# Kernel tuning notes

Measured on AMD Instinct MI355X. Metric: run time of the kernel, lower is better.

The kernel has to match this reference:

```python
import jax, jax.numpy as jnp
import numpy as np

B, T, N, D, H = 16, 96, 325, 64, 64
BS = 1e-09  # bias init constant

def _xavier(key, shape):
    fan_in, fan_out = shape
    limit = float(np.sqrt(6.0 / (fan_in + fan_out)))
    return jax.random.uniform(key, shape, jnp.float32, -limit, limit)

def setup_inputs() -> dict:
    key = jax.random.key(0)
    k = jax.random.split(key, 6)
    return {
        "x": jax.random.normal(k[0], (B, T, N, D), jnp.float32),
        "o_s": jax.random.normal(k[1], (B, T, N, D), jnp.float32),
        "U_x": _xavier(k[2], (D, 4 * H)),
        "V_x": _xavier(k[3], (H, 4 * H)),
        "b_x": jnp.full((4 * H,), BS, jnp.float32),
        "U_g": _xavier(k[4], (D, 2 * H)),
        "V_g": _xavier(k[5], (H, 2 * H)),
        "b_g": jnp.full((2 * H,), BS, jnp.float32),
    }

def reference(x, o_s, U_x, V_x, b_x, U_g, V_g, b_g):
    b, t, n, d = x.shape
    h = V_x.shape[0]
    ht0 = jnp.zeros((b, n, h), x.dtype)
    ct0 = jnp.zeros((b, n, h), x.dtype)

    def step(carry, inp):
        ht, ct = carry
        xt, ost = inp  # [b, n, d] each
        gates = xt @ U_x + ht @ V_x + b_x          # [b, n, 4h]
        gov = jax.nn.sigmoid(ost @ U_g + ht @ V_g + b_g)  # [b, n, 2h]
        ft = jax.nn.sigmoid(gates[..., :h])
        it = jax.nn.sigmoid(gates[..., h:2 * h])
        ot = jax.nn.sigmoid(gates[..., 2 * h:3 * h])
        ut = jax.nn.sigmoid(gates[..., 3 * h:])
        gov_f = gov[..., :h]
        gov_u = gov[..., h:]
        ct = gov_f * ft * ct + gov_u * it * ut
        ht = ot * jnp.tanh(ct)
        return (ht, ct), ht

    xs = (jnp.swapaxes(x, 0, 1), jnp.swapaxes(o_s, 0, 1))  # time-major [t, b, n, d]
    (ht, ct), hseq = jax.lax.scan(step, (ht0, ct0), xs)
    hidden_seq = jnp.swapaxes(hseq, 0, 1)  # [b, t, n, h]
    return hidden_seq, ht, ct
```

## Files before the change

kernel.cpp:

```cpp
#include <hip/hip_runtime.h>
#include <stdint.h>


#define TT 96
#define NNROW 325
#define STEP_OFS 20800
#define HT_OFS 31948800
#define CT_OFS 32281600

typedef __attribute__((ext_vector_type(8))) short short8;
typedef __attribute__((ext_vector_type(4))) float f32x4;

#define BAR() asm volatile("s_waitcnt lgkmcnt(0)\n\ts_barrier" ::: "memory")

__device__ __forceinline__ short f2bf(float f) {
    union { float f; uint32_t u; } v; v.f = f;
    uint32_t r = (v.u + 0x7FFFu + ((v.u >> 16) & 1u)) >> 16;
    return (short)(r & 0xFFFFu);
}
__device__ __forceinline__ float frcp(float x) { return __builtin_amdgcn_rcpf(x); }
__device__ __forceinline__ float ex2(float x)  { return __builtin_amdgcn_exp2f(x); }
__device__ __forceinline__ uint32_t cvtpk(float lo, float hi) {
    uint32_t r;
    asm("v_cvt_pk_bf16_f32 %0, %1, %2" : "=v"(r) : "v"(lo), "v"(hi));
    return r;
}

__global__ __launch_bounds__(256, 2)
void glstm_kernel(const float* __restrict__ x,
                  const float* __restrict__ o_s,
                  const float* __restrict__ U_x,
                  const float* __restrict__ V_x,
                  const float* __restrict__ b_x,
                  const float* __restrict__ U_g,
                  const float* __restrict__ V_g,
                  const float* __restrict__ b_g,
                  float* __restrict__ out)
{
    __shared__ __align__(16) short Xb[2][1024];
    __shared__ __align__(16) short Ob[2][1024];
    __shared__ __align__(16) short Hb[2][1024];

    const int tid  = threadIdx.x;
    const int g    = blockIdx.x;
    const int lane = tid & 63;
    const int w    = tid >> 6;
    const int q    = lane >> 4;
    const int ln   = lane & 15;

    short8 fWx[4][2], fWh[4][2], fGo[2][2], fGh[2][2];
    #pragma unroll
    for (int gt = 0; gt < 4; ++gt) {
        const int col = gt * 64 + w * 16 + ln;
        #pragma unroll
        for (int kb = 0; kb < 2; ++kb) {
            short8 a, b;
            #pragma unroll
            for (int j = 0; j < 8; ++j) {
                const int row = kb * 32 + q * 8 + j;
                a[j] = f2bf(U_x[(size_t)row * 256 + col]);
                b[j] = f2bf(V_x[(size_t)row * 256 + col]);
            }
            fWx[gt][kb] = a; fWh[gt][kb] = b;
        }
    }
    #pragma unroll
    for (int gt = 0; gt < 2; ++gt) {
        const int col = gt * 64 + w * 16 + ln;
        #pragma unroll
        for (int kb = 0; kb < 2; ++kb) {
            short8 a, b;
            #pragma unroll
            for (int j = 0; j < 8; ++j) {
                const int row = kb * 32 + q * 8 + j;
                a[j] = f2bf(U_g[(size_t)row * 128 + col]);
                b[j] = f2bf(V_g[(size_t)row * 128 + col]);
            }
            fGo[gt][kb] = a; fGh[gt][kb] = b;
        }
    }

    const int sm = tid >> 4;
    const int sd = tid & 15;
    const int srow = g * 16 + sm;
    const int sb = srow / NNROW;
    const int sn = srow - sb * NNROW;
    const size_t sbase = ((size_t)(sb * TT) * NNROW + sn) * 64 + sd * 4;
    const int stofs = (sm * 64 + (((sd >> 1) ^ (sm & 7)) << 3) + (sd & 1) * 4) * 2;

    const int o0 = ln * 128 + (((q    ) ^ (ln & 7)) << 4);
    const int o1 = ln * 128 + (((4 + q) ^ (ln & 7)) << 4);

    const int ch = w * 16 + ln;
    const float NL2E = -1.44269504f;
    const float nbf  = NL2E * b_x[ch];
    const float nbi  = NL2E * b_x[64  + ch];
    const float nbo  = NL2E * b_x[128 + ch];
    const float nbu  = NL2E * b_x[192 + ch];
    const float nbgf = NL2E * b_g[ch];
    const float nbgu = NL2E * b_g[64 + ch];

    size_t obase[4];
    int    fo[4];
    int    hofs[4];
    #pragma unroll
    for (int e = 0; e < 4; ++e) {
        const int m = q * 4 + e;
        const int row = g * 16 + m;
        const int b = row / NNROW;
        const int n = row - b * NNROW;
        obase[e] = ((size_t)(b * TT) * NNROW + n) * 64 + ch;
        fo[e]    = (b * NNROW + n) * 64 + ch;
        hofs[e]  = m * 64 + ((((ch >> 3) ^ (m & 7)) << 3) | (ch & 7));
    }
    float ct4[4] = {0.f, 0.f, 0.f, 0.f};

    {
        float4 x0 = *(const float4*)(x   + sbase);
        float4 s0 = *(const float4*)(o_s + sbase);
        uint2 sx; sx.x = cvtpk(x0.x, x0.y); sx.y = cvtpk(x0.z, x0.w);
        uint2 so; so.x = cvtpk(s0.x, s0.y); so.y = cvtpk(s0.z, s0.w);
        *(uint2*)((char*)&Xb[0][0] + stofs) = sx;
        *(uint2*)((char*)&Ob[0][0] + stofs) = so;
        uint2 z; z.x = 0u; z.y = 0u;
        *(uint2*)((char*)&Hb[0][0] + tid * 8) = z;
    }
    float4 xqA = *(const float4*)(x   + sbase + 1 * (size_t)STEP_OFS);
    float4 oqA = *(const float4*)(o_s + sbase + 1 * (size_t)STEP_OFS);
    float4 xqB = *(const float4*)(x   + sbase + 2 * (size_t)STEP_OFS);
    float4 oqB = *(const float4*)(o_s + sbase + 2 * (size_t)STEP_OFS);
    BAR();

    auto step = [&](int t, float4& xq, float4& oq) {
        const int p  = t & 1;
        const int pn = p ^ 1;
        const char* xb = (const char*)&Xb[p][0];
        const char* ob = (const char*)&Ob[p][0];
        const char* hb = (const char*)&Hb[p][0];
        const short8 ax0 = *(const short8*)(xb + o0);
        const short8 ax1 = *(const short8*)(xb + o1);
        const short8 ao0 = *(const short8*)(ob + o0);
        const short8 ao1 = *(const short8*)(ob + o1);
        const short8 ah0 = *(const short8*)(hb + o0);
        const short8 ah1 = *(const short8*)(hb + o1);

        f32x4 aF[4], aG[2];
        #pragma unroll
        for (int gt = 0; gt < 4; ++gt) {
            f32x4 acc = {0.f, 0.f, 0.f, 0.f};
            acc = __builtin_amdgcn_mfma_f32_16x16x32_bf16(ax0, fWx[gt][0], acc, 0, 0, 0);
            acc = __builtin_amdgcn_mfma_f32_16x16x32_bf16(ax1, fWx[gt][1], acc, 0, 0, 0);
            acc = __builtin_amdgcn_mfma_f32_16x16x32_bf16(ah0, fWh[gt][0], acc, 0, 0, 0);
            acc = __builtin_amdgcn_mfma_f32_16x16x32_bf16(ah1, fWh[gt][1], acc, 0, 0, 0);
            aF[gt] = acc;
        }
        #pragma unroll
        for (int gt = 0; gt < 2; ++gt) {
            f32x4 acc = {0.f, 0.f, 0.f, 0.f};
            acc = __builtin_amdgcn_mfma_f32_16x16x32_bf16(ao0, fGo[gt][0], acc, 0, 0, 0);
            acc = __builtin_amdgcn_mfma_f32_16x16x32_bf16(ao1, fGo[gt][1], acc, 0, 0, 0);
            acc = __builtin_amdgcn_mfma_f32_16x16x32_bf16(ah0, fGh[gt][0], acc, 0, 0, 0);
            acc = __builtin_amdgcn_mfma_f32_16x16x32_bf16(ah1, fGh[gt][1], acc, 0, 0, 0);
            aG[gt] = acc;
        }

        {
            uint2 sx; sx.x = cvtpk(xq.x, xq.y); sx.y = cvtpk(xq.z, xq.w);
            uint2 so; so.x = cvtpk(oq.x, oq.y); so.y = cvtpk(oq.z, oq.w);
            *(uint2*)((char*)&Xb[pn][0] + stofs) = sx;
            *(uint2*)((char*)&Ob[pn][0] + stofs) = so;
            int tn = t + 3; if (tn > TT - 1) tn = TT - 1;
            xq = *(const float4*)(x   + sbase + (size_t)tn * STEP_OFS);
            oq = *(const float4*)(o_s + sbase + (size_t)tn * STEP_OFS);
        }

        const size_t tofs = (size_t)t * STEP_OFS;
        float hv[4];
        #pragma unroll
        for (int e = 0; e < 4; ++e) {
            float ef  = ex2(fmaf(aF[0][e], NL2E, nbf));
            float ei  = ex2(fmaf(aF[1][e], NL2E, nbi));
            float eo  = ex2(fmaf(aF[2][e], NL2E, nbo));
            float eu  = ex2(fmaf(aF[3][e], NL2E, nbu));
            float egf = ex2(fmaf(aG[0][e], NL2E, nbgf));
            float egu = ex2(fmaf(aG[1][e], NL2E, nbgu));
            float rf = frcp((1.f + ef) * (1.f + egf));
            float ru = frcp(((1.f + ei) * (1.f + eu)) * (1.f + egu));
            float c  = fmaf(ct4[e], rf, ru);
            ct4[e] = c;
            float E  = ex2(c * 2.88539008f);
            float th = fmaf(-2.f, frcp(E + 1.f), 1.f);
            float h  = th * frcp(1.f + eo);
            hv[e] = h;
            out[obase[e] + tofs] = h;
            if (t == TT - 1) {
                out[HT_OFS + fo[e]] = h;
                out[CT_OFS + fo[e]] = c;
            }
        }

        {
            union { uint32_t u; short s[2]; } h01, h23;
            h01.u = cvtpk(hv[0], hv[1]);
            h23.u = cvtpk(hv[2], hv[3]);
            short* hn = &Hb[pn][0];
            hn[hofs[0]] = h01.s[0];
            hn[hofs[1]] = h01.s[1];
            hn[hofs[2]] = h23.s[0];
            hn[hofs[3]] = h23.s[1];
        }
        BAR();
    };

    for (int t = 0; t < TT; t += 2) {
        step(t,     xqA, oqA);
        step(t + 1, xqB, oqB);
    }
}

extern "C" void kernel_launch(void* const* d_in, const int* in_sizes, int n_in,
                              void* d_out, int out_size, void* d_ws, size_t ws_size,
                              hipStream_t stream) {
    const float* x   = (const float*)d_in[0];
    const float* o_s = (const float*)d_in[1];
    const float* U_x = (const float*)d_in[2];
    const float* V_x = (const float*)d_in[3];
    const float* b_x = (const float*)d_in[4];
    const float* U_g = (const float*)d_in[5];
    const float* V_g = (const float*)d_in[6];
    const float* b_g = (const float*)d_in[7];
    float* out = (float*)d_out;

    glstm_kernel<<<dim3(325), dim3(256), 0, stream>>>(x, o_s, U_x, V_x, b_x, U_g, V_g, b_g, out);
}
```

Baseline: 344.1 us.

## Process two row groups per block to interleave independent recurrences

Each block now handles two independent 16-row groups. Their MFMA chains and elementwise work interleave within one barrier per timestep, which aims to hide MFMA and exp latency through instruction-level parallelism. The grid halves to 163 blocks and launch bounds drop to one block per SIMD set. The elementwise maths is also rewritten with a single reciprocal for the cell update and a clamped tanh. In exchange, more of the GPU's CUs sit idle, and the last block computes a duplicated group (g1 is clamped to 324) that writes identical values.

```diff
diff --git a/kernel.cpp b/kernel.cpp
--- a/kernel.cpp
+++ b/kernel.cpp
@@ -26,7 +26,7 @@
     return r;
 }
 
-__global__ __launch_bounds__(256, 2)
+__global__ __launch_bounds__(256, 1)
 void glstm_kernel(const float* __restrict__ x,
                   const float* __restrict__ o_s,
                   const float* __restrict__ U_x,
@@ -37,12 +37,13 @@
                   const float* __restrict__ b_g,
                   float* __restrict__ out)
 {
-    __shared__ __align__(16) short Xb[2][1024];
-    __shared__ __align__(16) short Ob[2][1024];
-    __shared__ __align__(16) short Hb[2][1024];
-
-    const int tid  = threadIdx.x;
-    const int g    = blockIdx.x;
+    __shared__ __align__(16) short Xb[2][2][1024];
+    __shared__ __align__(16) short Ob[2][2][1024];
+    __shared__ __align__(16) short Hb[2][2][1024];
+
+    const int tid = threadIdx.x;
+    const int g0  = blockIdx.x * 2;
+    int g1 = g0 + 1; if (g1 > NNROW - 1) g1 = NNROW - 1;
     const int lane = tid & 63;
     const int w    = tid >> 6;
     const int q    = lane >> 4;
@@ -82,10 +83,12 @@
 
     const int sm = tid >> 4;
     const int sd = tid & 15;
-    const int srow = g * 16 + sm;
-    const int sb = srow / NNROW;
-    const int sn = srow - sb * NNROW;
-    const size_t sbase = ((size_t)(sb * TT) * NNROW + sn) * 64 + sd * 4;
+    const int sr0 = g0 * 16 + sm;
+    const int sb0 = sr0 / NNROW;
+    const size_t sbase0 = ((size_t)(sb0 * TT) * NNROW + (sr0 - sb0 * NNROW)) * 64 + sd * 4;
+    const int sr1 = g1 * 16 + sm;
+    const int sb1 = sr1 / NNROW;
+    const size_t sbase1 = ((size_t)(sb1 * TT) * NNROW + (sr1 - sb1 * NNROW)) * 64 + sd * 4;
     const int stofs = (sm * 64 + (((sd >> 1) ^ (sm & 7)) << 3) + (sd & 1) * 4) * 2;
 
     const int o0 = ln * 128 + (((q    ) ^ (ln & 7)) << 4);
@@ -100,121 +103,164 @@
     const float nbgf = NL2E * b_g[ch];
     const float nbgu = NL2E * b_g[64 + ch];
 
-    size_t obase[4];
-    int    fo[4];
-    int    hofs[4];
+    int obase0[4], obase1[4], hofs[4];
     #pragma unroll
     for (int e = 0; e < 4; ++e) {
         const int m = q * 4 + e;
-        const int row = g * 16 + m;
-        const int b = row / NNROW;
-        const int n = row - b * NNROW;
-        obase[e] = ((size_t)(b * TT) * NNROW + n) * 64 + ch;
-        fo[e]    = (b * NNROW + n) * 64 + ch;
-        hofs[e]  = m * 64 + ((((ch >> 3) ^ (m & 7)) << 3) | (ch & 7));
-    }
-    float ct4[4] = {0.f, 0.f, 0.f, 0.f};
+        {
+            const int row = g0 * 16 + m;
+            const int b = row / NNROW;
+            obase0[e] = ((b * TT) * NNROW + (row - b * NNROW)) * 64 + ch;
+        }
+        {
+            const int row = g1 * 16 + m;
+            const int b = row / NNROW;
+            obase1[e] = ((b * TT) * NNROW + (row - b * NNROW)) * 64 + ch;
+        }
+        hofs[e] = m * 64 + ((((ch >> 3) ^ (m & 7)) << 3) | (ch & 7));
+    }
+    float ct0[4] = {0.f, 0.f, 0.f, 0.f};
+    float ct1[4] = {0.f, 0.f, 0.f, 0.f};
 
     {
-        float4 x0 = *(const float4*)(x   + sbase);
-        float4 s0 = *(const float4*)(o_s + sbase);
-        uint2 sx; sx.x = cvtpk(x0.x, x0.y); sx.y = cvtpk(x0.z, x0.w);
-        uint2 so; so.x = cvtpk(s0.x, s0.y); so.y = cvtpk(s0.z, s0.w);
-        *(uint2*)((char*)&Xb[0][0] + stofs) = sx;
-        *(uint2*)((char*)&Ob[0][0] + stofs) = so;
+        float4 xa = *(const float4*)(x   + sbase0);
+        float4 sa = *(const float4*)(o_s + sbase0);
+        float4 xc = *(const float4*)(x   + sbase1);
+        float4 sc = *(const float4*)(o_s + sbase1);
+        uint2 v;
+        v.x = cvtpk(xa.x, xa.y); v.y = cvtpk(xa.z, xa.w);
+        *(uint2*)((char*)&Xb[0][0][0] + stofs) = v;
+        v.x = cvtpk(sa.x, sa.y); v.y = cvtpk(sa.z, sa.w);
+        *(uint2*)((char*)&Ob[0][0][0] + stofs) = v;
+        v.x = cvtpk(xc.x, xc.y); v.y = cvtpk(xc.z, xc.w);
+        *(uint2*)((char*)&Xb[1][0][0] + stofs) = v;
+        v.x = cvtpk(sc.x, sc.y); v.y = cvtpk(sc.z, sc.w);
+        *(uint2*)((char*)&Ob[1][0][0] + stofs) = v;
         uint2 z; z.x = 0u; z.y = 0u;
-        *(uint2*)((char*)&Hb[0][0] + tid * 8) = z;
-    }
-    float4 xqA = *(const float4*)(x   + sbase + 1 * (size_t)STEP_OFS);
-    float4 oqA = *(const float4*)(o_s + sbase + 1 * (size_t)STEP_OFS);
-    float4 xqB = *(const float4*)(x   + sbase + 2 * (size_t)STEP_OFS);
-    float4 oqB = *(const float4*)(o_s + sbase + 2 * (size_t)STEP_OFS);
+        *(uint2*)((char*)&Hb[0][0][0] + tid * 8) = z;
+        *(uint2*)((char*)&Hb[1][0][0] + tid * 8) = z;
+    }
+    float4 xq0 = *(const float4*)(x   + sbase0 + (size_t)STEP_OFS);
+    float4 oq0 = *(const float4*)(o_s + sbase0 + (size_t)STEP_OFS);
+    float4 xq1 = *(const float4*)(x   + sbase1 + (size_t)STEP_OFS);
+    float4 oq1 = *(const float4*)(o_s + sbase1 + (size_t)STEP_OFS);
     BAR();
 
-    auto step = [&](int t, float4& xq, float4& oq) {
+    for (int t = 0; t < TT; ++t) {
         const int p  = t & 1;
         const int pn = p ^ 1;
-        const char* xb = (const char*)&Xb[p][0];
-        const char* ob = (const char*)&Ob[p][0];
-        const char* hb = (const char*)&Hb[p][0];
-        const short8 ax0 = *(const short8*)(xb + o0);
-        const short8 ax1 = *(const short8*)(xb + o1);
-        const short8 ao0 = *(const short8*)(ob + o0);
-        const short8 ao1 = *(const short8*)(ob + o1);
-        const short8 ah0 = *(const short8*)(hb + o0);
-        const short8 ah1 = *(const short8*)(hb + o1);
-
-        f32x4 aF[4], aG[2];
+
+        const char* xb0 = (const char*)&Xb[0][0][0] + p * 2048;
+        const char* ob0 = (const char*)&Ob[0][0][0] + p * 2048;
+        const char* hb0 = (const char*)&Hb[0][0][0] + p * 2048;
+        const char* xb1 = (const char*)&Xb[1][0][0] + p * 2048;
+        const char* ob1 = (const char*)&Ob[1][0][0] + p * 2048;
+        const char* hb1 = (const char*)&Hb[1][0][0] + p * 2048;
+        const short8 ax00 = *(const short8*)(xb0 + o0);
+        const short8 ax01 = *(const short8*)(xb0 + o1);
+        const short8 ao00 = *(const short8*)(ob0 + o0);
+        const short8 ao01 = *(const short8*)(ob0 + o1);
+        const short8 ah00 = *(const short8*)(hb0 + o0);
+        const short8 ah01 = *(const short8*)(hb0 + o1);
+        const short8 ax10 = *(const short8*)(xb1 + o0);
+        const short8 ax11 = *(const short8*)(xb1 + o1);
+        const short8 ao10 = *(const short8*)(ob1 + o0);
+        const short8 ao11 = *(const short8*)(ob1 + o1);
+        const short8 ah10 = *(const short8*)(hb1 + o0);
+        const short8 ah11 = *(const short8*)(hb1 + o1);
+
+        f32x4 aF0[4], aG0[2], aF1[4], aG1[2];
         #pragma unroll
         for (int gt = 0; gt < 4; ++gt) {
-            f32x4 acc = {0.f, 0.f, 0.f, 0.f};
-            acc = __builtin_amdgcn_mfma_f32_16x16x32_bf16(ax0, fWx[gt][0], acc, 0, 0, 0);
-            acc = __builtin_amdgcn_mfma_f32_16x16x32_bf16(ax1, fWx[gt][1], acc, 0, 0, 0);
-            acc = __builtin_amdgcn_mfma_f32_16x16x32_bf16(ah0, fWh[gt][0], acc, 0, 0, 0);
-            acc = __builtin_amdgcn_mfma_f32_16x16x32_bf16(ah1, fWh[gt][1], acc, 0, 0, 0);
-            aF[gt] = acc;
+            f32x4 a = {0.f, 0.f, 0.f, 0.f};
+            a = __builtin_amdgcn_mfma_f32_16x16x32_bf16(ax00, fWx[gt][0], a, 0, 0, 0);
+            a = __builtin_amdgcn_mfma_f32_16x16x32_bf16(ax01, fWx[gt][1], a, 0, 0, 0);
+            a = __builtin_amdgcn_mfma_f32_16x16x32_bf16(ah00, fWh[gt][0], a, 0, 0, 0);
+            aF0[gt] = __builtin_amdgcn_mfma_f32_16x16x32_bf16(ah01, fWh[gt][1], a, 0, 0, 0);
+        }
+        #pragma unroll
+        for (int gt = 0; gt < 4; ++gt) {
+            f32x4 a = {0.f, 0.f, 0.f, 0.f};
+            a = __builtin_amdgcn_mfma_f32_16x16x32_bf16(ax10, fWx[gt][0], a, 0, 0, 0);
+            a = __builtin_amdgcn_mfma_f32_16x16x32_bf16(ax11, fWx[gt][1], a, 0, 0, 0);
+            a = __builtin_amdgcn_mfma_f32_16x16x32_bf16(ah10, fWh[gt][0], a, 0, 0, 0);
+            aF1[gt] = __builtin_amdgcn_mfma_f32_16x16x32_bf16(ah11, fWh[gt][1], a, 0, 0, 0);
         }
         #pragma unroll
         for (int gt = 0; gt < 2; ++gt) {
-            f32x4 acc = {0.f, 0.f, 0.f, 0.f};
-            acc = __builtin_amdgcn_mfma_f32_16x16x32_bf16(ao0, fGo[gt][0], acc, 0, 0, 0);
-            acc = __builtin_amdgcn_mfma_f32_16x16x32_bf16(ao1, fGo[gt][1], acc, 0, 0, 0);
-            acc = __builtin_amdgcn_mfma_f32_16x16x32_bf16(ah0, fGh[gt][0], acc, 0, 0, 0);
-            acc = __builtin_amdgcn_mfma_f32_16x16x32_bf16(ah1, fGh[gt][1], acc, 0, 0, 0);
-            aG[gt] = acc;
+            f32x4 a = {0.f, 0.f, 0.f, 0.f};
+            a = __builtin_amdgcn_mfma_f32_16x16x32_bf16(ao00, fGo[gt][0], a, 0, 0, 0);
+            a = __builtin_amdgcn_mfma_f32_16x16x32_bf16(ao01, fGo[gt][1], a, 0, 0, 0);
+            a = __builtin_amdgcn_mfma_f32_16x16x32_bf16(ah00, fGh[gt][0], a, 0, 0, 0);
+            aG0[gt] = __builtin_amdgcn_mfma_f32_16x16x32_bf16(ah01, fGh[gt][1], a, 0, 0, 0);
+        }
+        #pragma unroll
+        for (int gt = 0; gt < 2; ++gt) {
+            f32x4 a = {0.f, 0.f, 0.f, 0.f};
+            a = __builtin_amdgcn_mfma_f32_16x16x32_bf16(ao10, fGo[gt][0], a, 0, 0, 0);
+            a = __builtin_amdgcn_mfma_f32_16x16x32_bf16(ao11, fGo[gt][1], a, 0, 0, 0);
+            a = __builtin_amdgcn_mfma_f32_16x16x32_bf16(ah10, fGh[gt][0], a, 0, 0, 0);
+            aG1[gt] = __builtin_amdgcn_mfma_f32_16x16x32_bf16(ah11, fGh[gt][1], a, 0, 0, 0);
         }
 
         {
-            uint2 sx; sx.x = cvtpk(xq.x, xq.y); sx.y = cvtpk(xq.z, xq.w);
-            uint2 so; so.x = cvtpk(oq.x, oq.y); so.y = cvtpk(oq.z, oq.w);
-            *(uint2*)((char*)&Xb[pn][0] + stofs) = sx;
-            *(uint2*)((char*)&Ob[pn][0] + stofs) = so;
-            int tn = t + 3; if (tn > TT - 1) tn = TT - 1;
-            xq = *(const float4*)(x   + sbase + (size_t)tn * STEP_OFS);
-            oq = *(const float4*)(o_s + sbase + (size_t)tn * STEP_OFS);
-        }
-
-        const size_t tofs = (size_t)t * STEP_OFS;
-        float hv[4];
-        #pragma unroll
-        for (int e = 0; e < 4; ++e) {
-            float ef  = ex2(fmaf(aF[0][e], NL2E, nbf));
-            float ei  = ex2(fmaf(aF[1][e], NL2E, nbi));
-            float eo  = ex2(fmaf(aF[2][e], NL2E, nbo));
-            float eu  = ex2(fmaf(aF[3][e], NL2E, nbu));
-            float egf = ex2(fmaf(aG[0][e], NL2E, nbgf));
-            float egu = ex2(fmaf(aG[1][e], NL2E, nbgu));
-            float rf = frcp((1.f + ef) * (1.f + egf));
-            float ru = frcp(((1.f + ei) * (1.f + eu)) * (1.f + egu));
-            float c  = fmaf(ct4[e], rf, ru);
-            ct4[e] = c;
-            float E  = ex2(c * 2.88539008f);
-            float th = fmaf(-2.f, frcp(E + 1.f), 1.f);
-            float h  = th * frcp(1.f + eo);
-            hv[e] = h;
-            out[obase[e] + tofs] = h;
-            if (t == TT - 1) {
-                out[HT_OFS + fo[e]] = h;
-                out[CT_OFS + fo[e]] = c;
+            uint2 v;
+            v.x = cvtpk(xq0.x, xq0.y); v.y = cvtpk(xq0.z, xq0.w);
+            *(uint2*)((char*)&Xb[0][0][0] + pn * 2048 + stofs) = v;
+            v.x = cvtpk(oq0.x, oq0.y); v.y = cvtpk(oq0.z, oq0.w);
+            *(uint2*)((char*)&Ob[0][0][0] + pn * 2048 + stofs) = v;
+            v.x = cvtpk(xq1.x, xq1.y); v.y = cvtpk(xq1.z, xq1.w);
+            *(uint2*)((char*)&Xb[1][0][0] + pn * 2048 + stofs) = v;
+            v.x = cvtpk(oq1.x, oq1.y); v.y = cvtpk(oq1.z, oq1.w);
+            *(uint2*)((char*)&Ob[1][0][0] + pn * 2048 + stofs) = v;
+            int tn = t + 2; if (tn > TT - 1) tn = TT - 1;
+            xq0 = *(const float4*)(x   + sbase0 + (size_t)tn * STEP_OFS);
+            oq0 = *(const float4*)(o_s + sbase0 + (size_t)tn * STEP_OFS);
+            xq1 = *(const float4*)(x   + sbase1 + (size_t)tn * STEP_OFS);
+            oq1 = *(const float4*)(o_s + sbase1 + (size_t)tn * STEP_OFS);
+        }
+
+        const int tofs = t * STEP_OFS;
+        auto ew = [&](const f32x4* aF, const f32x4* aG, float* ct,
+                      const int* obase, int gg, short* hn) {
+            float hv[4];
+            #pragma unroll
+            for (int e = 0; e < 4; ++e) {
+                float ef  = ex2(fmaf(aF[0][e], NL2E, nbf));
+                float ei  = ex2(fmaf(aF[1][e], NL2E, nbi));
+                float eo  = ex2(fmaf(aF[2][e], NL2E, nbo));
+                float eu  = ex2(fmaf(aF[3][e], NL2E, nbu));
+                float egf = ex2(fmaf(aG[0][e], NL2E, nbgf));
+                float egu = ex2(fmaf(aG[1][e], NL2E, nbgu));
+                float P1 = (1.f + ef) * (1.f + egf);
+                float P2 = (1.f + ei) * (1.f + eu) * (1.f + egu);
+                float c  = fmaf(ct[e], P2, P1) * frcp(P1 * P2);
+                ct[e] = c;
+                float E  = ex2(fminf(c * 2.88539008f, 60.f));
+                float h  = (E - 1.f) * frcp((E + 1.f) * (1.f + eo));
+                hv[e] = h;
+                out[obase[e] + tofs] = h;
+                if (t == TT - 1) {
+                    const int m = q * 4 + e;
+                    const int row = gg * 16 + m;
+                    const int b = row / NNROW;
+                    const int f = (b * NNROW + (row - b * NNROW)) * 64 + ch;
+                    out[HT_OFS + f] = h;
+                    out[CT_OFS + f] = c;
+                }
             }
-        }
-
-        {
             union { uint32_t u; short s[2]; } h01, h23;
             h01.u = cvtpk(hv[0], hv[1]);
             h23.u = cvtpk(hv[2], hv[3]);
-            short* hn = &Hb[pn][0];
             hn[hofs[0]] = h01.s[0];
             hn[hofs[1]] = h01.s[1];
             hn[hofs[2]] = h23.s[0];
             hn[hofs[3]] = h23.s[1];
-        }
+        };
+        ew(aF0, aG0, ct0, obase0, g0, (short*)((char*)&Hb[0][0][0] + pn * 2048));
+        ew(aF1, aG1, ct1, obase1, g1, (short*)((char*)&Hb[1][0][0] + pn * 2048));
+
         BAR();
-    };
-
-    for (int t = 0; t < TT; t += 2) {
-        step(t,     xqA, oqA);
-        step(t + 1, xqB, oqB);
     }
 }
 
@@ -231,5 +277,5 @@
     const float* b_g = (const float*)d_in[7];
     float* out = (float*)d_out;
 
-    glstm_kernel<<<dim3(325), dim3(256), 0, stream>>>(x, o_s, U_x, V_x, b_x, U_g, V_g, b_g, out);
-}
+    glstm_kernel<<<dim3(163), dim3(256), 0, stream>>>(x, o_s, U_x, V_x, b_x, U_g, V_g, b_g, out);
+}
```

New measurement: 347.2 us. Within noise of the previous version (+0.9%).
